# Kernel optimization log

Hardware: AMD Instinct MI355X
Metric: run time of the kernel (lower is better)

The kernel has to match this reference:

```python
import jax, jax.numpy as jnp
import numpy as np
from jax import lax

HID = 256   # hidden_size
NN = 25     # n_nodes
T = 50      # seq_len
FIN = 16    # obs_length + 4
AS = 8      # action_space
HEADS = 5   # gat_head_num
E = 100     # edges per graph
B = 256     # batch


def setup_inputs() -> dict:
    key = jax.random.key(0)
    ks = jax.random.split(key, 32)
    s = 0.02
    def p(i, shape):
        return jax.random.normal(ks[i], shape, jnp.float32) * s
    return {
        "obs": jax.random.normal(ks[0], (B, NN, T, FIN), jnp.float32),
        "obs_map": jax.random.normal(ks[1], (B, 3, 84, 84), jnp.float32),
        "edges": jax.random.randint(ks[2], (B, 2, E), 0, NN),
        "edges_feature": jax.random.normal(ks[3], (B, E, 4), jnp.float32),
        "mlp_w": p(4, (FIN, HID)), "mlp_b": p(5, (HID,)),
        "c1_w": p(6, (32, 3, 8, 8)), "c1_b": p(7, (32,)),
        "c2_w": p(8, (64, 32, 4, 4)), "c2_b": p(9, (64,)),
        "c3_w": p(10, (64, 64, 3, 3)), "c3_b": p(11, (64,)),
        "fc_w": p(12, (3136, HID)), "fc_b": p(13, (HID,)),
        "gru_wih": p(14, (3 * HID, HID)), "gru_whh": p(15, (3 * HID, HID)),
        "gru_bih": p(16, (3 * HID,)), "gru_bhh": p(17, (3 * HID,)),
        "gat_wl": p(18, (HID, HEADS * HID)), "gat_bl": p(19, (HEADS * HID,)),
        "gat_wr": p(20, (HID, HEADS * HID)), "gat_br": p(21, (HEADS * HID,)),
        "gat_att": p(22, (HEADS, HID)), "gat_bias": p(23, (HID,)),
        "hid_w": p(24, (HID, HID)), "hid_b": p(25, (HID,)),
        "out_w": p(26, (HID, 1)), "out_b": p(27, (1,)),
        "adv_w": p(28, (HID, AS)), "adv_b": p(29, (AS,)),
    }


def _cnn(x, c1w, c1b, c2w, c2b, c3w, c3b, fcw, fcb):
    # Nature-CNN encoder: [B,3,84,84] -> [B,HID]
    dn = ('NCHW', 'OIHW', 'NCHW')
    h = jax.nn.relu(lax.conv_general_dilated(x, c1w, (4, 4), 'VALID', dimension_numbers=dn) + c1b[None, :, None, None])
    h = jax.nn.relu(lax.conv_general_dilated(h, c2w, (2, 2), 'VALID', dimension_numbers=dn) + c2b[None, :, None, None])
    h = jax.nn.relu(lax.conv_general_dilated(h, c3w, (1, 1), 'VALID', dimension_numbers=dn) + c3b[None, :, None, None])
    h = h.reshape(h.shape[0], -1)  # [B, 64*7*7]
    return jax.nn.relu(h @ fcw + fcb)


def _gru_last(x, wih, whh, bih, bhh):
    # torch nn.GRU (batch_first), return final hidden state [B,H]
    H = whh.shape[1]
    xg = x @ wih.T + bih  # precompute input gates [B,T,3H]
    def step(h, xg_t):
        hg = h @ whh.T + bhh
        xr, xz, xn = jnp.split(xg_t, 3, axis=-1)
        hr, hz, hn = jnp.split(hg, 3, axis=-1)
        r = jax.nn.sigmoid(xr + hr)
        z = jax.nn.sigmoid(xz + hz)
        n = jnp.tanh(xn + r * hn)
        return (1.0 - z) * n + z * h, None
    h0 = jnp.zeros((x.shape[0], H), x.dtype)
    hT, _ = lax.scan(step, h0, jnp.swapaxes(xg, 0, 1))
    return hT


def _gat(x, ei, wl, bl, wr, br, att, gbias):
    # GATv2Conv (concat=False): one graph, x [N,H], ei [2,E'] incl. self loops
    n = x.shape[0]
    heads, ch = att.shape
    src, dst = ei[0], ei[1]
    gl = (x @ wl + bl).reshape(n, heads, ch)
    gr = (x @ wr + br).reshape(n, heads, ch)
    e = jax.nn.leaky_relu(gl[src] + gr[dst], 0.2)          # [E',H,C]
    score = jnp.einsum('ehc,hc->eh', e, att)               # [E',H]
    m = jax.ops.segment_max(score, dst, num_segments=n)
    ex = jnp.exp(score - m[dst])
    den = jax.ops.segment_sum(ex, dst, num_segments=n)
    alpha = ex / den[dst]                                   # softmax per dst node
    out = jax.ops.segment_sum(alpha[:, :, None] * gl[src], dst, num_segments=n)
    return out.mean(axis=1) + gbias, alpha                  # mean over heads (concat=False)


def reference(obs, obs_map, edges, edges_feature, mlp_w, mlp_b, c1_w, c1_b, c2_w, c2_b, c3_w, c3_b, fc_w, fc_b, gru_wih, gru_whh, gru_bih, gru_bhh, gat_wl, gat_bl, gat_wr, gat_br, gat_att, gat_bias, hid_w, hid_b, out_w, out_b, adv_w, adv_b):
    bsz, n = obs.shape[0], obs.shape[1]
    n_edges = edges.shape[2]
    target_emb = _cnn(obs_map, c1_w, c1_b, c2_w, c2_b, c3_w, c3_b, fc_w, fc_b)[:, None, :]
    nbrs = obs[:, 1:].reshape(bsz * (n - 1), obs.shape[2], obs.shape[3])
    nbrs_emb = jax.nn.relu(nbrs @ mlp_w + mlp_b)            # MLP_rnn (Linear+ReLU)
    nbrs_h = _gru_last(nbrs_emb, gru_wih, gru_whh, gru_bih, gru_bhh).reshape(bsz, n - 1, -1)
    node_emb = jnp.concatenate([target_emb, nbrs_h], axis=1)  # [B,N,HID]
    loops = jnp.broadcast_to(jnp.arange(n)[None, None, :], (bsz, 2, n))
    ei = jnp.concatenate([edges, loops], axis=2)            # PyG add_self_loops (appended)
    gat_out, alpha = jax.vmap(lambda xg, eg: _gat(xg, eg, gat_wl, gat_bl, gat_wr, gat_br, gat_att, gat_bias))(node_emb, ei)
    att_w = alpha[:, : n_edges + 1].mean(axis=-1)           # matches att_weights[:-n_nodes+1].mean(axis=1)
    h = jax.nn.relu(gat_out[:, 0] @ hid_w + hid_b)          # only node-0 feature used
    v = h @ out_w + out_b
    adv = h @ adv_w + adv_b
    q = v + (adv - adv.mean(axis=-1, keepdims=True))        # dueling head
    return q, att_w
```

## Files before the change

### kernel.cpp

```cpp
#include <hip/hip_runtime.h>
#include <cstdint>

typedef __attribute__((ext_vector_type(8))) __bf16 bf16x8;
typedef __attribute__((ext_vector_type(4))) float f32x4;
typedef __attribute__((ext_vector_type(4))) unsigned int uint4v;
typedef __attribute__((ext_vector_type(2))) unsigned int uint2v;
typedef __attribute__((ext_vector_type(4))) float float4v;
typedef __attribute__((ext_vector_type(2))) long long2v;

__device__ __forceinline__ unsigned short f2bf(float x){
  union { float f; unsigned u; } v; v.f = x;
  unsigned r = v.u + 0x7FFFu + ((v.u >> 16) & 1u);
  return (unsigned short)(r >> 16);
}
__device__ __forceinline__ float bf2f(unsigned short h){
  union { unsigned u; float f; } v; v.u = ((unsigned)h) << 16;
  return v.f;
}
__device__ __forceinline__ float bflo(unsigned u){
  union { unsigned x; float f; } v; v.x = u << 16; return v.f;
}
__device__ __forceinline__ float bfhi(unsigned u){
  union { unsigned x; float f; } v; v.x = u & 0xFFFF0000u; return v.f;
}
__device__ __forceinline__ f32x4 MFMA16(bf16x8 a, bf16x8 b, f32x4 c){
  return __builtin_amdgcn_mfma_f32_16x16x32_bf16(a, b, c, 0, 0, 0);
}
__device__ __forceinline__ f32x4 MFMA8(long a, long b, f32x4 c){
  return __builtin_amdgcn_mfma_f32_16x16x32_fp8_fp8(a, b, c, 0, 0, 0);
}
__device__ __forceinline__ unsigned char f2fp8(float x){
  int p = __builtin_amdgcn_cvt_pk_fp8_f32(x, x, 0, false);
  return (unsigned char)(p & 0xFF);
}

__global__ __launch_bounds__(256) void prep_k(
    const float* __restrict__ wih, const float* __restrict__ whh,
    const float* __restrict__ wl, const float* __restrict__ wr,
    const float* __restrict__ bl, const float* __restrict__ br,
    const float* __restrict__ fcw, const float* __restrict__ mlpw,
    unsigned char* __restrict__ wfrag8, unsigned short* __restrict__ mlpfrag,
    unsigned short* __restrict__ wlrT, unsigned short* __restrict__ fcwT,
    float* __restrict__ blbr){
  int i = blockIdx.x*256 + threadIdx.x;
  if (i < 393216){
    int b16 = i & 15;
    int l   = (i >> 4) & 63;
    int chunk = i >> 10;
    int wkp = chunk / 6;
    int mg  = chunk - 6*wkp;
    int w = wkp >> 2, kkp = wkp & 3;
    int ks = b16 >> 3, e = b16 & 7;
    int kk = kkp*2 + ks;
    int mat = mg / 3, g = mg - 3*(mg/3);
    int n = g*256 + w*16 + (l & 15);
    int k = kk*32 + (l >> 4)*8 + e;
    float v = 16.f * (mat ? whh[n*256 + k] : wih[n*256 + k]);
    wfrag8[i] = f2fp8(v);
    return;
  }
  i -= 393216;
  if (i < 8192){
    int w = i >> 9;
    int r4 = i & 511;
    int l = r4 >> 3, e = r4 & 7;
    int n = w*16 + (l & 15);
    int k = (l >> 4)*8 + e;
    mlpfrag[i] = (k < 16) ? f2bf(mlpw[k*256 + n]) : (unsigned short)0;
    return;
  }
  i -= 8192;
  if (i < 655360){
    int n = i >> 8, k = i & 255;
    float v = (n < 1280) ? wl[k*1280 + n] : wr[k*1280 + (n-1280)];
    wlrT[i] = f2bf(v); return;
  }
  i -= 655360;
  if (i < 802816){
    int n = i / 3136, k = i - n*3136;
    fcwT[i] = f2bf(fcw[k*256 + n]); return;
  }
  i -= 802816;
  if (i < 2560){
    blbr[i] = (i < 1280) ? bl[i] : br[i-1280];
  }
}

__global__ __launch_bounds__(256) void conv1_k(const float* __restrict__ in,
              const float* __restrict__ w, const float* __restrict__ bias,
              unsigned short* __restrict__ out){
  __shared__ float in_s[3][24][84];
  __shared__ float w_s[32][3][8][8];
  __shared__ float b_s[32];
  int bid = blockIdx.x; int b = bid >> 2, q = bid & 3;
  int t = threadIdx.x;
  for (int idx = t; idx < 3*24*84; idx += 256){
    int ic = idx / (24*84); int rem = idx - ic*(24*84);
    int iy = rem / 84, ix = rem - iy*84;
    in_s[ic][iy][ix] = in[((size_t)(b*3+ic)*84 + (q*20 + iy))*84 + ix];
  }
  for (int idx = t; idx < 32*192; idx += 256) ((float*)w_s)[idx] = w[idx];
  if (t < 32) b_s[t] = bias[t];
  __syncthreads();
  for (int p = t; p < 800; p += 256){
    int oc = p / 25; int rem = p - oc*25;
    int oy = rem / 5, og = rem - oy*5;
    float a0=b_s[oc],a1=b_s[oc],a2=b_s[oc],a3=b_s[oc];
    #pragma unroll
    for (int ic=0;ic<3;ic++){
      #pragma unroll
      for (int ky=0;ky<8;ky++){
        const float* row = &in_s[ic][oy*4+ky][og*16];
        float s[20];
        #pragma unroll
        for (int cc=0;cc<20;cc++) s[cc]=row[cc];
        const float* wp = &w_s[oc][ic][ky][0];
        #pragma unroll
        for (int kx=0;kx<8;kx++){
          float wv = wp[kx];
          a0 += s[kx]*wv; a1 += s[4+kx]*wv; a2 += s[8+kx]*wv; a3 += s[12+kx]*wv;
        }
      }
    }
    size_t ob = ((size_t)(b*32+oc)*20 + (q*5+oy))*20 + og*4;
    out[ob+0]=f2bf(fmaxf(a0,0.f)); out[ob+1]=f2bf(fmaxf(a1,0.f));
    out[ob+2]=f2bf(fmaxf(a2,0.f)); out[ob+3]=f2bf(fmaxf(a3,0.f));
  }
}

__global__ __launch_bounds__(256) void conv2_k(const unsigned short* __restrict__ in,
              const float* __restrict__ w, const float* __restrict__ bias,
              unsigned short* __restrict__ out){
  __shared__ unsigned short in_s[32][20][20];
  __shared__ float w_s[16][32][4][4];
  __shared__ float b_s[16];
  int bid = blockIdx.x; int b = bid >> 2, h = bid & 3;
  int t = threadIdx.x;
  for (int idx = t; idx < 32*400; idx += 256) ((unsigned short*)in_s)[idx] = in[(size_t)b*12800 + idx];
  for (int idx = t; idx < 16*512; idx += 256) ((float*)w_s)[idx] = w[h*8192 + idx];
  if (t < 16) b_s[t] = bias[h*16 + t];
  __syncthreads();
  for (int p = t; p < 432; p += 256){
    int ocl = p / 27; int rem = p - ocl*27;
    int oy = rem / 3, og = rem - oy*3;
    float a0=b_s[ocl],a1=b_s[ocl],a2=b_s[ocl];
    #pragma unroll 4
    for (int ic=0;ic<32;ic++){
      #pragma unroll
      for (int ky=0;ky<4;ky++){
        const unsigned short* row = &in_s[ic][oy*2+ky][og*6];
        float s[8];
        #pragma unroll
        for (int cc=0;cc<8;cc++) s[cc]=bf2f(row[cc]);
        const float* wp = &w_s[ocl][ic][ky][0];
        #pragma unroll
        for (int kx=0;kx<4;kx++){
          float wv = wp[kx];
          a0 += s[kx]*wv; a1 += s[2+kx]*wv; a2 += s[4+kx]*wv;
        }
      }
    }
    size_t ob = ((size_t)(b*64 + h*16+ocl)*9 + oy)*9 + og*3;
    out[ob+0]=f2bf(fmaxf(a0,0.f)); out[ob+1]=f2bf(fmaxf(a1,0.f)); out[ob+2]=f2bf(fmaxf(a2,0.f));
  }
}

__global__ __launch_bounds__(256) void conv3_k(const unsigned short* __restrict__ in,
              const float* __restrict__ w, const float* __restrict__ bias,
              unsigned short* __restrict__ out){
  __shared__ unsigned short in_s[64][9][9];
  __shared__ float w_s[16][64][3][3];
  __shared__ float b_s[16];
  int bid = blockIdx.x; int b = bid >> 2, h = bid & 3;
  int t = threadIdx.x;
  for (int idx = t; idx < 64*81; idx += 256) ((unsigned short*)in_s)[idx] = in[(size_t)b*5184 + idx];
  for (int idx = t; idx < 16*576; idx += 256) ((float*)w_s)[idx] = w[h*9216 + idx];
  if (t < 16) b_s[t] = bias[h*16 + t];
  __syncthreads();
  for (int p = t; p < 224; p += 256){
    int ocl = p / 14; int rem = p - ocl*14;
    int oy = rem >> 1, og = rem & 1;
    int ox0 = og*4; int nx = og ? 3 : 4;
    float a[4]; a[0]=a[1]=a[2]=a[3]=b_s[ocl];
    for (int ic=0;ic<64;ic++){
      #pragma unroll
      for (int ky=0;ky<3;ky++){
        const unsigned short* row = &in_s[ic][oy+ky][ox0];
        float s[6];
        #pragma unroll
        for (int cc=0;cc<6;cc++) s[cc] = (ox0+cc < 9) ? bf2f(row[cc]) : 0.f;
        const float* wp = &w_s[ocl][ic][ky][0];
        #pragma unroll
        for (int kx=0;kx<3;kx++){
          float wv = wp[kx];
          #pragma unroll
          for (int jj=0;jj<4;jj++) a[jj] += s[jj+kx]*wv;
        }
      }
    }
    size_t ob = (size_t)b*3136 + (h*16+ocl)*49 + oy*7 + ox0;
    #pragma unroll
    for (int jj=0;jj<4;jj++) if (jj < nx) out[ob+jj] = f2bf(fmaxf(a[jj],0.f));
  }
}

__global__ __launch_bounds__(256) void gemm_k(const unsigned short* __restrict__ A,
              const unsigned short* __restrict__ B, const float* __restrict__ bias,
              unsigned short* __restrict__ C, int K, int ldc, int rowmul, int relu, int Nblk){
  __shared__ __align__(16) unsigned short As[64*32];
  __shared__ __align__(16) unsigned short Bs[64*32];
  int bid = blockIdx.x;
  int nb = bid % Nblk, mb = bid / Nblk;
  int t = threadIdx.x;
  int w = t >> 6, l = t & 63, lr = l & 15, lh = l >> 4;
  int sr = t >> 2, sq = t & 3;
  f32x4 acc[4];
  #pragma unroll
  for (int i=0;i<4;i++) acc[i] = (f32x4){0.f,0.f,0.f,0.f};
  int nkk = K >> 5;
  const size_t a_row = (size_t)(mb*64 + sr)*K;
  const size_t b_row = (size_t)(nb*64 + sr)*K;
  for (int kk=0;kk<nkk;kk++){
    uint4v av = *(const uint4v*)&A[a_row + kk*32 + sq*8];
    uint4v bv = *(const uint4v*)&B[b_row + kk*32 + sq*8];
    __syncthreads();
    *(uint4v*)((char*)As + ((sr*64 + sq*16) ^ ((sr&3)<<4))) = av;
    *(uint4v*)((char*)Bs + ((sr*64 + sq*16) ^ ((sr&3)<<4))) = bv;
    __syncthreads();
    int brow = w*16 + lr;
    bf16x8 bfr = *(const bf16x8*)((char*)Bs + ((brow*64 + lh*16) ^ ((brow&3)<<4)));
    #pragma unroll
    for (int mt=0;mt<4;mt++){
      int arow = mt*16 + lr;
      bf16x8 afr = *(const bf16x8*)((char*)As + ((arow*64 + lh*16) ^ ((arow&3)<<4)));
      acc[mt] = MFMA16(afr, bfr, acc[mt]);
    }
  }
  int col = nb*64 + w*16 + lr;
  float bn = bias[col];
  #pragma unroll
  for (int mt=0;mt<4;mt++){
    #pragma unroll
    for (int r=0;r<4;r++){
      int row = mb*64 + mt*16 + lh*4 + r;
      float v = acc[mt][r] + bn;
      if (relu) v = fmaxf(v, 0.f);
      C[(size_t)row*rowmul*ldc + col] = f2bf(v);
    }
  }
}

__global__ __launch_bounds__(1024, 4) void gru_k(const float* __restrict__ obs,
              const unsigned char* __restrict__ wfrag8,
              const unsigned short* __restrict__ mlpfrag,
              const float* __restrict__ mlpb,
              const float* __restrict__ bih, const float* __restrict__ bhh,
              unsigned short* __restrict__ nemb){
  __shared__ __align__(16) unsigned short obsA[1024];
  __shared__ __align__(16) unsigned char e8_0[8192];
  __shared__ __align__(16) unsigned char e8_1[8192];
  __shared__ __align__(16) unsigned char h8[8192];

  const int t = threadIdx.x, blk = blockIdx.x;
  obsA[t & 1023] = 0;
  for (int j = t; j < 8192; j += 1024) h8[j] = 0;

  const int w = t >> 6, l = t & 63, lr = l & 15, lh = l >> 4;
  const int jcol = w*16 + lr;
  const float bR  = bih[jcol]     + bhh[jcol];
  const float bZ  = bih[256+jcol] + bhh[256+jcol];
  const float bXN = bih[512+jcol];
  const float bHN = bhh[512+jcol];
  const float bMb = mlpb[jcol];
  const bf16x8 bMLP = *(const bf16x8*)(mlpfrag + w*512 + l*8);

  const unsigned char* wb8 = wfrag8 + w*24576 + l*16;

  const int srow = t >> 2, sk4 = t & 3;
  int rrS = blk*32 + srow; int bS = rrS/24, ndS = 1 + (rrS - bS*24);
  const float* obase4 = obs + (size_t)(bS*25 + ndS)*800 + sk4*4;
  const int obyte = (srow*64 + sk4*8) ^ ((srow&3)<<4);

  const int a8off = lr*256 + lh*8;
  const int xr8 = lr << 3;
  const int o16 = lh*16;
  const int oa0b = (lr*64 + o16) ^ ((lr&3)<<4);
  const int oa1b = ((16+lr)*64 + o16) ^ ((lr&3)<<4);
  const int hw0 = jcol;
  const float S = 1.f/256.f;

  f32x4 hs0 = (f32x4){0.f,0.f,0.f,0.f};
  f32x4 hs1 = (f32x4){0.f,0.f,0.f,0.f};

#define EMB_COMPUTE(DST) { \
  f32x4 e0 = (f32x4){0.f,0.f,0.f,0.f}, e1 = (f32x4){0.f,0.f,0.f,0.f}; \
  bf16x8 oa0 = *(const bf16x8*)((char*)obsA + oa0b); \
  bf16x8 oa1 = *(const bf16x8*)((char*)obsA + oa1b); \
  e0 = MFMA16(oa0, bMLP, e0); \
  e1 = MFMA16(oa1, bMLP, e1); \
  _Pragma("unroll") \
  for (int r=0;r<4;r++){ \
    int m = lh*4 + r; \
    (DST)[(m*256 + hw0) ^ ((m&15)<<3)] = f2fp8(fmaxf(e0[r] + bMb, 0.f)*16.f); \
    int m2 = m + 16; \
    (DST)[(m2*256 + hw0) ^ ((m2&15)<<3)] = f2fp8(fmaxf(e1[r] + bMb, 0.f)*16.f); \
  } }

  __syncthreads();
  if (t < 128){
    float4v ov = *(const float4v*)(obase4);
    uint2v pk;
    pk[0] = (unsigned)f2bf(ov[0]) | ((unsigned)f2bf(ov[1]) << 16);
    pk[1] = (unsigned)f2bf(ov[2]) | ((unsigned)f2bf(ov[3]) << 16);
    *(uint2v*)((char*)obsA + obyte) = pk;
  }
  __syncthreads();
  EMB_COMPUTE(e8_0)
  __syncthreads();

  for (int step=0; step<50; step++){
    const unsigned char* ebuf = (step & 1) ? e8_1 : e8_0;
    unsigned char* nbuf = (step & 1) ? e8_0 : e8_1;
    const bool stg = (t < 128) && (step < 49);
    float4v ov;
    if (stg) ov = *(const float4v*)(obase4 + (size_t)(step+1)*16);

    f32x4 aR0=(f32x4){0,0,0,0}, aR1=(f32x4){0,0,0,0};
    f32x4 aZ0=(f32x4){0,0,0,0}, aZ1=(f32x4){0,0,0,0};
    f32x4 aN0=(f32x4){0,0,0,0}, aN1=(f32x4){0,0,0,0};
    f32x4 aM0=(f32x4){0,0,0,0}, aM1=(f32x4){0,0,0,0};
    __builtin_amdgcn_s_setprio(1);
    #pragma unroll 2
    for (int kkp=0;kkp<4;kkp++){
      const unsigned char* wk8 = wb8 + kkp*6144;
      long2v wIR = *(const long2v*)(wk8);
      long2v wIZ = *(const long2v*)(wk8 + 1024);
      long2v wIN = *(const long2v*)(wk8 + 2048);
      long2v wHR = *(const long2v*)(wk8 + 3072);
      long2v wHZ = *(const long2v*)(wk8 + 4096);
      long2v wHN = *(const long2v*)(wk8 + 5120);
      {
        int kk = kkp*2;
        int ab = a8off + kk*32;
        long eA0 = *(const long*)(ebuf + (ab ^ xr8));
        long eA1 = *(const long*)(ebuf + ((ab + 4096) ^ xr8));
        long hA0 = *(const long*)(h8 + (ab ^ xr8));
        long hA1 = *(const long*)(h8 + ((ab + 4096) ^ xr8));
        aR0 = MFMA8(eA0, wIR[0], aR0);  aR0 = MFMA8(hA0, wHR[0], aR0);
        aR1 = MFMA8(eA1, wIR[0], aR1);  aR1 = MFMA8(hA1, wHR[0], aR1);
        aZ0 = MFMA8(eA0, wIZ[0], aZ0);  aZ0 = MFMA8(hA0, wHZ[0], aZ0);
        aZ1 = MFMA8(eA1, wIZ[0], aZ1);  aZ1 = MFMA8(hA1, wHZ[0], aZ1);
        aN0 = MFMA8(eA0, wIN[0], aN0);  aN1 = MFMA8(eA1, wIN[0], aN1);
        aM0 = MFMA8(hA0, wHN[0], aM0);  aM1 = MFMA8(hA1, wHN[0], aM1);
      }
      {
        int kk = kkp*2 + 1;
        int ab = a8off + kk*32;
        long eA0 = *(const long*)(ebuf + (ab ^ xr8));
        long eA1 = *(const long*)(ebuf + ((ab + 4096) ^ xr8));
        long hA0 = *(const long*)(h8 + (ab ^ xr8));
        long hA1 = *(const long*)(h8 + ((ab + 4096) ^ xr8));
        aR0 = MFMA8(eA0, wIR[1], aR0);  aR0 = MFMA8(hA0, wHR[1], aR0);
        aR1 = MFMA8(eA1, wIR[1], aR1);  aR1 = MFMA8(hA1, wHR[1], aR1);
        aZ0 = MFMA8(eA0, wIZ[1], aZ0);  aZ0 = MFMA8(hA0, wHZ[1], aZ0);
        aZ1 = MFMA8(eA1, wIZ[1], aZ1);  aZ1 = MFMA8(hA1, wHZ[1], aZ1);
        aN0 = MFMA8(eA0, wIN[1], aN0);  aN1 = MFMA8(eA1, wIN[1], aN1);
        aM0 = MFMA8(hA0, wHN[1], aM0);  aM1 = MFMA8(hA1, wHN[1], aM1);
      }
    }
    __builtin_amdgcn_s_setprio(0);
    if (stg){
      uint2v pk;
      pk[0] = (unsigned)f2bf(ov[0]) | ((unsigned)f2bf(ov[1]) << 16);
      pk[1] = (unsigned)f2bf(ov[2]) | ((unsigned)f2bf(ov[3]) << 16);
      *(uint2v*)((char*)obsA + obyte) = pk;
    }
    __syncthreads();
    if (step < 49){
      EMB_COMPUTE(nbuf)
    }
    #pragma unroll
    for (int mt=0;mt<2;mt++){
      f32x4 vR = mt ? aR1 : aR0;
      f32x4 vZ = mt ? aZ1 : aZ0;
      f32x4 vN = mt ? aN1 : aN0;
      f32x4 vM = mt ? aM1 : aM0;
      #pragma unroll
      for (int r=0;r<4;r++){
        float rp = vR[r]*S + bR;
        float zp = vZ[r]*S + bZ;
        float xn = vN[r]*S + bXN;
        float hn = vM[r]*S + bHN;
        float rg = 1.f/(1.f + __expf(-rp));
        float zg = 1.f/(1.f + __expf(-zp));
        float arg = xn + rg*hn;
        float e2 = __expf(2.f*arg);
        float nv = (e2 - 1.f)/(e2 + 1.f);
        float hold = mt ? hs1[r] : hs0[r];
        float hnew = (1.f - zg)*nv + zg*hold;
        if (mt) hs1[r] = hnew; else hs0[r] = hnew;
        int m = mt*16 + lh*4 + r;
        h8[(m*256 + hw0) ^ ((m&15)<<3)] = f2fp8(hnew*16.f);
        if (step == 49){
          int rr = blk*32 + m; int b = rr/24; int nd = 1 + (rr - b*24);
          nemb[(size_t)(b*25+nd)*256 + jcol] = f2bf(hnew);
        }
      }
    }
    __syncthreads();
  }
#undef EMB_COMPUTE
}

__global__ __launch_bounds__(256) void gat_k(const int* __restrict__ edges,
              const unsigned short* __restrict__ glgr,
              const float* __restrict__ att, const float* __restrict__ gbias,
              const float* __restrict__ hidw, const float* __restrict__ hidb,
              const float* __restrict__ outw, const float* __restrict__ outb,
              const float* __restrict__ advw, const float* __restrict__ advb,
              float* __restrict__ out){
  __shared__ int src_s[125], dst_s[125];
  __shared__ __align__(16) float att_s[1280];
  __shared__ float sc[125][5], al[125][5];
  __shared__ float mx[25][5], dn[25][5];
  __shared__ float g0[256], hh[256];
  __shared__ float adv_s[8], v_s;
  __shared__ int e0[125]; __shared__ int ne0;

  int b = blockIdx.x, t = threadIdx.x;
  if (t < 100){ src_s[t] = edges[b*200 + t]; dst_s[t] = edges[b*200 + 100 + t]; }
  else if (t < 125){ src_s[t] = t - 100; dst_s[t] = t - 100; }
  for (int j = t; j < 1280; j += 256) att_s[j] = att[j];
  __syncthreads();
  if (t == 0){ int c = 0; for (int e=0;e<125;e++) if (dst_s[e]==0) e0[c++]=e; ne0 = c; }
  const unsigned short* gbase = glgr + (size_t)b*25*2560;
  for (int p = t; p < 625; p += 256){
    int e = p/5, h = p - 5*(p/5);
    const unsigned short* glp = gbase + src_s[e]*2560 + h*256;
    const unsigned short* grp = gbase + dst_s[e]*2560 + 1280 + h*256;
    const float* ap = &att_s[h*256];
    float acc = 0.f;
    #pragma unroll 4
    for (int c=0;c<256;c+=8){
      uint4v gu = *(const uint4v*)&glp[c];
      uint4v ru = *(const uint4v*)&grp[c];
      #pragma unroll
      for (int q=0;q<4;q++){
        float s0 = bflo(gu[q]) + bflo(ru[q]);
        float s1 = bfhi(gu[q]) + bfhi(ru[q]);
        s0 = (s0 > 0.f) ? s0 : 0.2f*s0;
        s1 = (s1 > 0.f) ? s1 : 0.2f*s1;
        acc += s0*ap[c+2*q] + s1*ap[c+2*q+1];
      }
    }
    sc[e][h] = acc;
  }
  __syncthreads();
  if (t < 125){
    int j = t/5, h = t - 5*(t/5);
    float m = -1e30f;
    for (int e=0;e<125;e++) if (dst_s[e]==j) m = fmaxf(m, sc[e][h]);
    float d = 0.f;
    for (int e=0;e<125;e++) if (dst_s[e]==j) d += __expf(sc[e][h]-m);
    mx[j][h] = m; dn[j][h] = d;
  }
  __syncthreads();
  for (int p = t; p < 625; p += 256){
    int e = p/5, h = p - 5*(p/5);
    int dd = dst_s[e];
    al[e][h] = __expf(sc[e][h] - mx[dd][h]) / dn[dd][h];
  }
  __syncthreads();
  if (t < 101){
    out[2048 + b*101 + t] = (al[t][0]+al[t][1]+al[t][2]+al[t][3]+al[t][4])*0.2f;
  }
  {
    float acc = 0.f;
    for (int x=0;x<ne0;x++){
      int e = e0[x]; int s = src_s[e];
      const unsigned short* glp = gbase + s*2560 + t;
      #pragma unroll
      for (int h=0;h<5;h++) acc += al[e][h]*bf2f(glp[h*256]);
    }
    g0[t] = acc*0.2f + gbias[t];
  }
  __syncthreads();
  {
    float acc = hidb[t];
    for (int k=0;k<256;k++) acc += g0[k]*hidw[k*256+t];
    hh[t] = fmaxf(acc, 0.f);
  }
  __syncthreads();
  if (t < 8){
    float acc = advb[t];
    for (int k=0;k<256;k++) acc += hh[k]*advw[k*8+t];
    adv_s[t] = acc;
  } else if (t == 8){
    float acc = outb[0];
    for (int k=0;k<256;k++) acc += hh[k]*outw[k];
    v_s = acc;
  }
  __syncthreads();
  if (t < 8){
    float m = adv_s[0]+adv_s[1]+adv_s[2]+adv_s[3]+adv_s[4]+adv_s[5]+adv_s[6]+adv_s[7];
    out[b*8+t] = v_s + adv_s[t] - m*0.125f;
  }
}

extern "C" void kernel_launch(void* const* d_in, const int* in_sizes, int n_in,
                              void* d_out, int out_size, void* d_ws, size_t ws_size,
                              hipStream_t stream){
  const float* obs     = (const float*)d_in[0];
  const float* obs_map = (const float*)d_in[1];
  const int*   edges   = (const int*)d_in[2];
  const float* mlp_w = (const float*)d_in[4];
  const float* mlp_b = (const float*)d_in[5];
  const float* c1w = (const float*)d_in[6];  const float* c1b = (const float*)d_in[7];
  const float* c2w = (const float*)d_in[8];  const float* c2b = (const float*)d_in[9];
  const float* c3w = (const float*)d_in[10]; const float* c3b = (const float*)d_in[11];
  const float* fcw = (const float*)d_in[12]; const float* fcb = (const float*)d_in[13];
  const float* wih = (const float*)d_in[14]; const float* whh = (const float*)d_in[15];
  const float* bih = (const float*)d_in[16]; const float* bhh = (const float*)d_in[17];
  const float* gwl = (const float*)d_in[18]; const float* gbl = (const float*)d_in[19];
  const float* gwr = (const float*)d_in[20]; const float* gbr = (const float*)d_in[21];
  const float* gatt = (const float*)d_in[22]; const float* gbias = (const float*)d_in[23];
  const float* hidw = (const float*)d_in[24]; const float* hidb = (const float*)d_in[25];
  const float* outw = (const float*)d_in[26]; const float* outb = (const float*)d_in[27];
  const float* advw = (const float*)d_in[28]; const float* advb = (const float*)d_in[29];
  float* out = (float*)d_out;
  char* ws = (char*)d_ws;

  unsigned short* c1o  = (unsigned short*)(ws + 0);
  unsigned short* c2o  = (unsigned short*)(ws + 6553600);
  unsigned short* c3o  = (unsigned short*)(ws + 9207808);
  unsigned short* glgr = (unsigned short*)(ws + 0);
  size_t o = 32768000;
  unsigned short* nemb    = (unsigned short*)(ws + o); o += 3276800;
  unsigned char*  wfrag8  = (unsigned char*)(ws + o);  o += 393216;
  unsigned short* mlpfrag = (unsigned short*)(ws + o); o += 16384;
  unsigned short* wlrT    = (unsigned short*)(ws + o); o += 1310720;
  unsigned short* fcwT    = (unsigned short*)(ws + o); o += 1605632;
  float* blbr             = (float*)(ws + o); o += 10240;

  prep_k<<<7274, 256, 0, stream>>>(wih, whh, gwl, gwr, gbl, gbr, fcw, mlp_w, wfrag8, mlpfrag, wlrT, fcwT, blbr);
  conv1_k<<<1024, 256, 0, stream>>>(obs_map, c1w, c1b, c1o);
  conv2_k<<<1024, 256, 0, stream>>>(c1o, c2w, c2b, c2o);
  conv3_k<<<1024, 256, 0, stream>>>(c2o, c3w, c3b, c3o);
  gemm_k<<<16, 256, 0, stream>>>(c3o, fcwT, fcb, nemb, 3136, 256, 25, 1, 4);
  gru_k<<<192, 1024, 0, stream>>>(obs, wfrag8, mlpfrag, mlp_b, bih, bhh, nemb);
  gemm_k<<<4000, 256, 0, stream>>>(nemb, wlrT, blbr, glgr, 256, 2560, 1, 0, 40);
  gat_k<<<256, 256, 0, stream>>>(edges, glgr, gatt, gbias, hidw, hidb, outw, outb, advw, advb, out);
}
```

Measured before the change: 821.4 us.

## Split-K the CNN fc GEMM, pad GRU LDS, fully unroll GRU k-loop

The 16-block fc GEMM (K=3136) becomes a 7-way split-K kernel over 112 blocks that writes fp32 partials, followed by a reduction kernel that adds bias, applies ReLU and writes bf16 node embeddings. The GRU kernel gets a 60 KB dummy LDS array and a waves-per-eu attribute that limit occupancy to one block per CU, and its inner k-loop is fully unrolled. The split-K is meant to fill the GPU instead of leaving most CUs idle on a long serial K loop. The LDS padding and unrolling are meant to give each GRU block more registers or less contention, at the cost of occupancy and an extra launch plus partial-sum traffic.

```diff
diff --git a/kernel.cpp b/kernel.cpp
--- a/kernel.cpp
+++ b/kernel.cpp
@@ -250,7 +250,61 @@
   }
 }
 
-__global__ __launch_bounds__(1024, 4) void gru_k(const float* __restrict__ obs,
+__global__ __launch_bounds__(256) void gemm_fc_k(const unsigned short* __restrict__ A,
+              const unsigned short* __restrict__ B, float* __restrict__ P){
+  __shared__ __align__(16) unsigned short As[64*32];
+  __shared__ __align__(16) unsigned short Bs[64*32];
+  int bid = blockIdx.x;
+  int s = bid % 7, tile = bid / 7;
+  int nb = tile & 3, mb = tile >> 2;
+  int t = threadIdx.x;
+  int w = t >> 6, l = t & 63, lr = l & 15, lh = l >> 4;
+  int sr = t >> 2, sq = t & 3;
+  f32x4 acc[4];
+  #pragma unroll
+  for (int i=0;i<4;i++) acc[i] = (f32x4){0.f,0.f,0.f,0.f};
+  const int K = 3136;
+  const size_t a_row = (size_t)(mb*64 + sr)*K;
+  const size_t b_row = (size_t)(nb*64 + sr)*K;
+  for (int kk = s*14; kk < s*14 + 14; kk++){
+    uint4v av = *(const uint4v*)&A[a_row + kk*32 + sq*8];
+    uint4v bv = *(const uint4v*)&B[b_row + kk*32 + sq*8];
+    __syncthreads();
+    *(uint4v*)((char*)As + ((sr*64 + sq*16) ^ ((sr&3)<<4))) = av;
+    *(uint4v*)((char*)Bs + ((sr*64 + sq*16) ^ ((sr&3)<<4))) = bv;
+    __syncthreads();
+    int brow = w*16 + lr;
+    bf16x8 bfr = *(const bf16x8*)((char*)Bs + ((brow*64 + lh*16) ^ ((brow&3)<<4)));
+    #pragma unroll
+    for (int mt=0;mt<4;mt++){
+      int arow = mt*16 + lr;
+      bf16x8 afr = *(const bf16x8*)((char*)As + ((arow*64 + lh*16) ^ ((arow&3)<<4)));
+      acc[mt] = MFMA16(afr, bfr, acc[mt]);
+    }
+  }
+  int col = nb*64 + w*16 + lr;
+  #pragma unroll
+  for (int mt=0;mt<4;mt++){
+    #pragma unroll
+    for (int r=0;r<4;r++){
+      int row = mb*64 + mt*16 + lh*4 + r;
+      P[(size_t)s*65536 + row*256 + col] = acc[mt][r];
+    }
+  }
+}
+
+__global__ __launch_bounds__(256) void fc_red_k(const float* __restrict__ P,
+              const float* __restrict__ fcb, unsigned short* __restrict__ nemb){
+  int idx = blockIdx.x*256 + threadIdx.x;
+  int row = idx >> 8, col = idx & 255;
+  float sum = fcb[col];
+  #pragma unroll
+  for (int k=0;k<7;k++) sum += P[k*65536 + idx];
+  nemb[(size_t)row*25*256 + col] = f2bf(fmaxf(sum, 0.f));
+}
+
+__global__ __launch_bounds__(1024, 4) __attribute__((amdgpu_waves_per_eu(4,4)))
+void gru_k(const float* __restrict__ obs,
               const unsigned char* __restrict__ wfrag8,
               const unsigned short* __restrict__ mlpfrag,
               const float* __restrict__ mlpb,
@@ -260,8 +314,10 @@
   __shared__ __align__(16) unsigned char e8_0[8192];
   __shared__ __align__(16) unsigned char e8_1[8192];
   __shared__ __align__(16) unsigned char h8[8192];
+  __shared__ char lds_pad[60000];
 
   const int t = threadIdx.x, blk = blockIdx.x;
+  if (blk == 0x7fffffff) ((volatile char*)lds_pad)[t] = 1;
   obsA[t & 1023] = 0;
   for (int j = t; j < 8192; j += 1024) h8[j] = 0;
 
@@ -330,7 +386,7 @@
     f32x4 aN0=(f32x4){0,0,0,0}, aN1=(f32x4){0,0,0,0};
     f32x4 aM0=(f32x4){0,0,0,0}, aM1=(f32x4){0,0,0,0};
     __builtin_amdgcn_s_setprio(1);
-    #pragma unroll 2
+    #pragma unroll
     for (int kkp=0;kkp<4;kkp++){
       const unsigned char* wk8 = wb8 + kkp*6144;
       long2v wIR = *(const long2v*)(wk8);
@@ -533,6 +589,7 @@
   unsigned short* c1o  = (unsigned short*)(ws + 0);
   unsigned short* c2o  = (unsigned short*)(ws + 6553600);
   unsigned short* c3o  = (unsigned short*)(ws + 9207808);
+  float*          fcpart = (float*)(ws + 16000000);
   unsigned short* glgr = (unsigned short*)(ws + 0);
   size_t o = 32768000;
   unsigned short* nemb    = (unsigned short*)(ws + o); o += 3276800;
@@ -546,7 +603,8 @@
   conv1_k<<<1024, 256, 0, stream>>>(obs_map, c1w, c1b, c1o);
   conv2_k<<<1024, 256, 0, stream>>>(c1o, c2w, c2b, c2o);
   conv3_k<<<1024, 256, 0, stream>>>(c2o, c3w, c3b, c3o);
-  gemm_k<<<16, 256, 0, stream>>>(c3o, fcwT, fcb, nemb, 3136, 256, 25, 1, 4);
+  gemm_fc_k<<<112, 256, 0, stream>>>(c3o, fcwT, fcpart);
+  fc_red_k<<<256, 256, 0, stream>>>(fcpart, fcb, nemb);
   gru_k<<<192, 1024, 0, stream>>>(obs, wfrag8, mlpfrag, mlp_b, bih, bhh, nemb);
   gemm_k<<<4000, 256, 0, stream>>>(nemb, wlrT, blbr, glgr, 256, 2560, 1, 0, 40);
   gat_k<<<256, 256, 0, stream>>>(edges, glgr, gatt, gbias, hidw, hidb, outw, outb, advw, advb, out);
```

New measurement: 1.166 ms. +41.9%, slower.
